# Performance work log

Measured on AMD Instinct MI355X. Metric: run time of the kernel, lower is better.

Reference implementation:

```python
import jax, jax.numpy as jnp
import numpy as np

N, E, D_IN, D_OUT = 100000, 3200000, 128, 128


def setup_inputs() -> dict:
    key = jax.random.key(0)
    ks = jax.random.split(key, 6)
    return {
        "x": jax.random.normal(ks[0], (N, D_IN), dtype=jnp.float32),
        "row": jax.random.randint(ks[1], (E,), 0, N),
        "col": jax.random.randint(ks[2], (E,), 0, N),
        "W0": jax.random.normal(ks[3], (D_OUT, D_IN), dtype=jnp.float32) * (1.0 / np.sqrt(D_IN)),
        "b0": jnp.zeros((D_OUT,), jnp.float32),
        "W1": jax.random.normal(ks[4], (D_OUT, D_IN), dtype=jnp.float32) * (1.0 / np.sqrt(D_IN)),
        "b1": jnp.zeros((D_OUT,), jnp.float32),
        "att": jax.random.normal(ks[5], (2 * D_OUT,), dtype=jnp.float32) * 0.1,
        "scale0": jnp.ones((D_OUT,), jnp.float32),
        "offset0": jnp.zeros((D_OUT,), jnp.float32),
        "scale1": jnp.ones((D_OUT,), jnp.float32),
        "offset1": jnp.zeros((D_OUT,), jnp.float32),
    }


def _norm(f, scale, offset):
    # per-node normalization over feature dim (bias='norm' branch)
    m = jnp.mean(f, axis=1, keepdims=True)
    v = jnp.var(f, axis=1, keepdims=True) + 1e-9
    return (f - m) * scale * jax.lax.rsqrt(v) + offset


def reference(x, row, col, W0, b0, W1, b1, att, scale0, offset0, scale1, offset1):
    d = W0.shape[0]
    # order-0 (self) and order-1 (neighbor) feature transforms, act='relu'
    h0 = jax.nn.relu(x @ W0.T + b0)  # [N, d]
    h1 = jax.nn.relu(x @ W1.T + b1)  # [N, d]
    # unnormalized GAT attention (no softmax), LeakyReLU(0.2)
    a_self = jax.nn.leaky_relu(h0 @ att[:d], negative_slope=0.2)   # [N]
    a_neigh = jax.nn.leaky_relu(h1 @ att[d:], negative_slope=0.2)  # [N]
    e = a_self[row] + a_neigh[col]                                 # [E]
    # SpMM: out[i] = sum_{(i,j) in edges} e_ij * h1[j]
    agg = jax.ops.segment_sum(e[:, None] * h1[col], row, num_segments=h0.shape[0])
    # batch-norm style normalization per head, then mean-aggregate over orders
    out = _norm(h0, scale0, offset0) + _norm(agg, scale1, offset1)
    return out
```

## Files before the change

kernel.cpp:

```cpp
#include <hip/hip_runtime.h>
#include <hip/hip_bf16.h>

constexpr int D = 128;
constexpr int BUCKET_SHIFT = 7;
constexpr int BUCKET_CAP_LOG2 = 13;
constexpr int BUCKET_CAP = 1 << BUCKET_CAP_LOG2;
typedef __hip_bfloat16 bf16;

__global__ __launch_bounds__(256) void k_gemm(
    const float* __restrict__ x,
    const float* __restrict__ W0, const float* __restrict__ b0,
    const float* __restrict__ W1, const float* __restrict__ b1,
    const float* __restrict__ att,
    float* __restrict__ h0, bf16* __restrict__ h1b,
    float* __restrict__ a_self, float* __restrict__ a_neigh, int N)
{
  constexpr int XS_STRIDE = 132;
  constexpr int WS_STRIDE = 68;
  __shared__ float xs_t[64 * XS_STRIDE];
  __shared__ float ws_t[64 * WS_STRIDE];

  const int t  = threadIdx.x;
  const int nb = blockIdx.x;
  const int fb = blockIdx.y;
  const int n0 = nb * 128;

  const float* __restrict__ W    = (fb < 2) ? W0 : W1;
  const float* __restrict__ bias = (fb < 2) ? b0 : b1;
  float* __restrict__ adest      = (fb < 2) ? a_self : a_neigh;
  const int frow0 = (fb & 1) * 64;

  const int tf = t & 15;
  const int tn = t >> 4;

  const int x_nq = t >> 1;
  const int x_kq = t & 1;
  const int w_f  = t >> 2;
  const int w_kq = t & 3;

  float acc[8][4];
#pragma unroll
  for (int i = 0; i < 8; ++i)
#pragma unroll
    for (int j = 0; j < 4; ++j) acc[i][j] = 0.0f;

  const bool x_ok = (n0 + x_nq) < N;
  const float* xrow = x + (size_t)(n0 + x_nq) * D;
  const float* wrow = W + (size_t)(frow0 + w_f) * D;

  for (int c = 0; c < 2; ++c) {
    const int k0 = c * 64;
    if (c) __syncthreads();

#pragma unroll
    for (int i = 0; i < 8; ++i) {
      const int k = x_kq * 32 + i * 4;
      float4 v = x_ok ? *reinterpret_cast<const float4*>(xrow + k0 + k)
                      : make_float4(0.f, 0.f, 0.f, 0.f);
      xs_t[(k + 0) * XS_STRIDE + x_nq] = v.x;
      xs_t[(k + 1) * XS_STRIDE + x_nq] = v.y;
      xs_t[(k + 2) * XS_STRIDE + x_nq] = v.z;
      xs_t[(k + 3) * XS_STRIDE + x_nq] = v.w;
    }
#pragma unroll
    for (int i = 0; i < 4; ++i) {
      const int k = w_kq * 4 + i * 16;
      float4 v = *reinterpret_cast<const float4*>(wrow + k0 + k);
      ws_t[(k + 0) * WS_STRIDE + w_f] = v.x;
      ws_t[(k + 1) * WS_STRIDE + w_f] = v.y;
      ws_t[(k + 2) * WS_STRIDE + w_f] = v.z;
      ws_t[(k + 3) * WS_STRIDE + w_f] = v.w;
    }
    __syncthreads();

#pragma unroll 4
    for (int k = 0; k < 64; ++k) {
      const float4 a0 = *reinterpret_cast<const float4*>(&xs_t[k * XS_STRIDE + tn * 4]);
      const float4 a1 = *reinterpret_cast<const float4*>(&xs_t[k * XS_STRIDE + 64 + tn * 4]);
      const float4 bvec = *reinterpret_cast<const float4*>(&ws_t[k * WS_STRIDE + tf * 4]);
      const float av[8] = {a0.x, a0.y, a0.z, a0.w, a1.x, a1.y, a1.z, a1.w};
      const float bv[4] = {bvec.x, bvec.y, bvec.z, bvec.w};
#pragma unroll
      for (int i = 0; i < 8; ++i)
#pragma unroll
        for (int j = 0; j < 4; ++j)
          acc[i][j] = fmaf(av[i], bv[j], acc[i][j]);
    }
  }

  const float4 b4 = *reinterpret_cast<const float4*>(&bias[frow0 + tf * 4]);
  const float4 at4 = *reinterpret_cast<const float4*>(
      &att[(fb < 2 ? 0 : 128) + frow0 + tf * 4]);
#pragma unroll
  for (int i = 0; i < 8; ++i) {
    const int nq = (i < 4) ? (tn * 4 + i) : (64 + tn * 4 + (i - 4));
    const int node = n0 + nq;
    float4 r;
    r.x = fmaxf(acc[i][0] + b4.x, 0.0f);
    r.y = fmaxf(acc[i][1] + b4.y, 0.0f);
    r.z = fmaxf(acc[i][2] + b4.z, 0.0f);
    r.w = fmaxf(acc[i][3] + b4.w, 0.0f);
    float pdot = r.x * at4.x + r.y * at4.y + r.z * at4.z + r.w * at4.w;
#pragma unroll
    for (int m2 = 1; m2 < 16; m2 <<= 1) pdot += __shfl_xor(pdot, m2, 16);
    if (node < N) {
      if (fb < 2) {
        *reinterpret_cast<float4*>(&h0[(size_t)node * D + frow0 + tf * 4]) = r;
      } else {
        bf16 p[4] = {__float2bfloat16(r.x), __float2bfloat16(r.y),
                     __float2bfloat16(r.z), __float2bfloat16(r.w)};
        *reinterpret_cast<ushort4*>(&h1b[(size_t)node * D + frow0 + tf * 4]) =
            *reinterpret_cast<const ushort4*>(p);
      }
      if (tf == 0) atomicAdd(&adest[node], pdot);
    }
  }
}

__global__ __launch_bounds__(512) void k_binA(
    const int* __restrict__ row, const int* __restrict__ col,
    int* __restrict__ bukCnt, unsigned* __restrict__ buf1, int E, int NBUK)
{
  constexpr int EPB = 16384;
  __shared__ int hist[1024];
  __shared__ int base[1024];
  const int t = threadIdx.x;
  const int e0 = blockIdx.x * EPB;
  const int e1 = min(e0 + EPB, E);

  for (int i = t; i < 1024; i += 512) hist[i] = 0;
  __syncthreads();
  for (int e = e0 + t; e < e1; e += 512)
    atomicAdd(&hist[row[e] >> BUCKET_SHIFT], 1);
  __syncthreads();
  for (int bk = t; bk < NBUK; bk += 512) {
    int c = hist[bk];
    base[bk] = (c > 0) ? atomicAdd(&bukCnt[bk], c) : 0;
  }
  __syncthreads();
  for (int i = t; i < 1024; i += 512) hist[i] = 0;
  __syncthreads();
  for (int e = e0 + t; e < e1; e += 512) {
    int r = row[e];
    int c = col[e];
    int bk = r >> BUCKET_SHIFT;
    int pos = base[bk] + atomicAdd(&hist[bk], 1);
    if (pos < BUCKET_CAP)
      buf1[((size_t)bk << BUCKET_CAP_LOG2) + pos] =
          ((unsigned)c << BUCKET_SHIFT) | (unsigned)(r & 127);
  }
}

__global__ __launch_bounds__(1024) void k_scanB(
    const int* __restrict__ bukCnt, int* __restrict__ bukBase, int NBUK)
{
  __shared__ int sd[1024];
  const int t = threadIdx.x;
  const int v = (t < NBUK) ? min(bukCnt[t], BUCKET_CAP) : 0;
  sd[t] = v;
  __syncthreads();
  for (int d2 = 1; d2 < 1024; d2 <<= 1) {
    int o = (t >= d2) ? sd[t - d2] : 0;
    __syncthreads();
    sd[t] += o;
    __syncthreads();
  }
  if (t < NBUK) bukBase[t] = sd[t] - v;
}

__global__ __launch_bounds__(256) void k_fine(
    const unsigned* __restrict__ buf1,
    const int* __restrict__ bukCnt, const int* __restrict__ bukBase,
    int* __restrict__ offs, int* __restrict__ cnt,
    int* __restrict__ colS, int N)
{
  __shared__ int lhist[128], lbase[128], lcur[128];
  __shared__ int sd[256];
  const int b = blockIdx.x;
  const int t = threadIdx.x;
  const int rstart = b << BUCKET_SHIFT;
  const int n = min(bukCnt[b], BUCKET_CAP);
  const unsigned* src = buf1 + ((size_t)b << BUCKET_CAP_LOG2);

  if (t < 128) lhist[t] = 0;
  __syncthreads();
  for (int i = t; i < n; i += 256) atomicAdd(&lhist[src[i] & 127u], 1);
  __syncthreads();
  const int v = (t < 128) ? lhist[t] : 0;
  sd[t] = v;
  __syncthreads();
  for (int d2 = 1; d2 < 128; d2 <<= 1) {
    int o = (t >= d2) ? sd[t - d2] : 0;
    __syncthreads();
    sd[t] += o;
    __syncthreads();
  }
  if (t < 128) {
    const int gbase = bukBase[b] + (sd[t] - v);
    lbase[t] = gbase;
    lcur[t] = 0;
    const int r = rstart + t;
    if (r < N) { offs[r] = gbase; cnt[r] = v; }
  }
  __syncthreads();
  for (int i = t; i < n; i += 256) {
    unsigned w = src[i];
    int r = (int)(w & 127u);
    int pos = lbase[r] + atomicAdd(&lcur[r], 1);
    colS[pos] = (int)(w >> BUCKET_SHIFT);
  }
}

__global__ __launch_bounds__(128) void k_agg(
    const float* __restrict__ h0, const bf16* __restrict__ h1b,
    const float* __restrict__ a_self, const float* __restrict__ a_neigh,
    const int* __restrict__ offs, const int* __restrict__ cnt,
    const int* __restrict__ colS,
    const float* __restrict__ scale0, const float* __restrict__ offset0,
    const float* __restrict__ scale1, const float* __restrict__ offset1,
    float* __restrict__ out, int N)
{
  constexpr int CHUNK = 128;
  __shared__ int2  je[CHUNK];
  __shared__ float red[4];
  __shared__ float aggs[128];
  const int i = blockIdx.x;
  const int d = threadIdx.x;
  const int w = d >> 6;
  const int l = d & 63;

  const float h0v = h0[(size_t)i * D + d];

  float a = h0v, b = h0v * h0v;
#pragma unroll
  for (int o = 32; o; o >>= 1) { a += __shfl_down(a, o, 64); b += __shfl_down(b, o, 64); }
  if ((d & 63) == 0) { red[d >> 6] = a; red[2 + (d >> 6)] = b; }
  __syncthreads();
  const float sum0 = red[0] + red[1], sq0 = red[2] + red[3];

  const int start = offs[i];
  const int deg = cnt[i];
  const float asr = a_self[i];
  const float asv = asr > 0.0f ? asr : 0.2f * asr;

  float acc0 = 0.0f, acc1 = 0.0f;
  const char* h1base = reinterpret_cast<const char*>(h1b) + l * 4;

  for (int c0 = 0; c0 < deg; c0 += CHUNK) {
    const int m = min(CHUNK, deg - c0);
    __syncthreads();
    if (d < m) {
      int j = colS[start + c0 + d];
      float an = a_neigh[j];
      an = an > 0.0f ? an : 0.2f * an;
      je[d] = make_int2(j << 8, __float_as_int(asv + an));
    }
    __syncthreads();
    int k = w;
    for (; k + 6 < m; k += 8) {
      int2 p0 = je[k], p1 = je[k + 2], p2 = je[k + 4], p3 = je[k + 6];
      unsigned u0 = *reinterpret_cast<const unsigned*>(h1base + p0.x);
      unsigned u1 = *reinterpret_cast<const unsigned*>(h1base + p1.x);
      unsigned u2 = *reinterpret_cast<const unsigned*>(h1base + p2.x);
      unsigned u3 = *reinterpret_cast<const unsigned*>(h1base + p3.x);
      float w0 = __int_as_float(p0.y), w1 = __int_as_float(p1.y);
      float w2 = __int_as_float(p2.y), w3 = __int_as_float(p3.y);
      acc0 = fmaf(w0, __uint_as_float(u0 << 16), acc0);
      acc1 = fmaf(w0, __uint_as_float(u0 & 0xffff0000u), acc1);
      acc0 = fmaf(w1, __uint_as_float(u1 << 16), acc0);
      acc1 = fmaf(w1, __uint_as_float(u1 & 0xffff0000u), acc1);
      acc0 = fmaf(w2, __uint_as_float(u2 << 16), acc0);
      acc1 = fmaf(w2, __uint_as_float(u2 & 0xffff0000u), acc1);
      acc0 = fmaf(w3, __uint_as_float(u3 << 16), acc0);
      acc1 = fmaf(w3, __uint_as_float(u3 & 0xffff0000u), acc1);
    }
    for (; k < m; k += 2) {
      int2 p = je[k];
      unsigned u = *reinterpret_cast<const unsigned*>(h1base + p.x);
      float wg = __int_as_float(p.y);
      acc0 = fmaf(wg, __uint_as_float(u << 16), acc0);
      acc1 = fmaf(wg, __uint_as_float(u & 0xffff0000u), acc1);
    }
  }

  if (w == 0) *reinterpret_cast<float2*>(&aggs[2 * l]) = make_float2(acc0, acc1);
  __syncthreads();
  if (w == 1) {
    float2 p = *reinterpret_cast<float2*>(&aggs[2 * l]);
    *reinterpret_cast<float2*>(&aggs[2 * l]) = make_float2(p.x + acc0, p.y + acc1);
  }
  __syncthreads();
  const float agg = aggs[d];

  float a1 = agg, b1 = agg * agg;
#pragma unroll
  for (int o = 32; o; o >>= 1) { a1 += __shfl_down(a1, o, 64); b1 += __shfl_down(b1, o, 64); }
  __syncthreads();
  if ((d & 63) == 0) { red[d >> 6] = a1; red[2 + (d >> 6)] = b1; }
  __syncthreads();
  const float sum1 = red[0] + red[1], sq1 = red[2] + red[3];

  const float inv = 1.0f / 128.0f;
  const float m0 = sum0 * inv;
  const float v0 = sq0 * inv - m0 * m0 + 1e-9f;
  const float m1 = sum1 * inv;
  const float v1 = sq1 * inv - m1 * m1 + 1e-9f;
  const float n0v = (h0v - m0) * scale0[d] * rsqrtf(v0) + offset0[d];
  const float n1v = (agg - m1) * scale1[d] * rsqrtf(v1) + offset1[d];
  out[(size_t)i * D + d] = n0v + n1v;
}

extern "C" void kernel_launch(void* const* d_in, const int* in_sizes, int n_in,
                              void* d_out, int out_size, void* d_ws, size_t ws_size,
                              hipStream_t stream)
{
  const float* x       = (const float*)d_in[0];
  const int*   row     = (const int*)d_in[1];
  const int*   col     = (const int*)d_in[2];
  const float* W0      = (const float*)d_in[3];
  const float* b0      = (const float*)d_in[4];
  const float* W1      = (const float*)d_in[5];
  const float* b1      = (const float*)d_in[6];
  const float* att     = (const float*)d_in[7];
  const float* scale0  = (const float*)d_in[8];
  const float* offset0 = (const float*)d_in[9];
  const float* scale1  = (const float*)d_in[10];
  const float* offset1 = (const float*)d_in[11];

  const int N = in_sizes[0] / D;
  const int E = in_sizes[1];
  const int NBUK = (N + 127) >> BUCKET_SHIFT;

  char* ws = (char*)d_ws;
  size_t off = 0;
  auto alloc = [&](size_t bytes) -> void* {
    void* p = ws + off;
    off += (bytes + 511) & ~size_t(511);
    return p;
  };

  float*    h0      = (float*)d_out;
  bf16*     h1b     = (bf16*)alloc((size_t)N * D * sizeof(bf16));
  float*    a_self  = (float*)alloc((size_t)N * sizeof(float));
  float*    a_neigh = (float*)alloc((size_t)N * sizeof(float));
  int*      cnt     = (int*)alloc((size_t)N * sizeof(int));
  int*      offs    = (int*)alloc((size_t)N * sizeof(int));
  int*      bukCnt  = (int*)alloc((size_t)NBUK * sizeof(int));
  int*      bukBase = (int*)alloc((size_t)NBUK * sizeof(int));
  unsigned* buf1    = (unsigned*)alloc(((size_t)NBUK << BUCKET_CAP_LOG2) * sizeof(unsigned));
  int*      colS    = (int*)alloc((size_t)E * sizeof(int));

  hipMemsetAsync(a_self, 0, (size_t)N * sizeof(float), stream);
  hipMemsetAsync(a_neigh, 0, (size_t)N * sizeof(float), stream);
  hipMemsetAsync(bukCnt, 0, (size_t)NBUK * sizeof(int), stream);

  dim3 ggrid((N + 127) / 128, 4);
  k_gemm<<<ggrid, 256, 0, stream>>>(x, W0, b0, W1, b1, att, h0, h1b,
                                    a_self, a_neigh, N);
  const int NBLKA = (E + 16383) / 16384;
  k_binA<<<NBLKA, 512, 0, stream>>>(row, col, bukCnt, buf1, E, NBUK);
  k_scanB<<<1, 1024, 0, stream>>>(bukCnt, bukBase, NBUK);
  k_fine<<<NBUK, 256, 0, stream>>>(buf1, bukCnt, bukBase, offs, cnt, colS, N);
  k_agg<<<N, 128, 0, stream>>>(h0, h1b, a_self, a_neigh, offs, cnt, colS,
                               scale0, offset0, scale1, offset1, (float*)d_out, N);
}
```

Measured before the change: 331.4 us.

## Sort edges into row-by-column-segment runs and aggregate 64 rows per block

Edges are now bucketed per 64 rows and sub-binned by row group, column segment and row, so each wave walks runs of edges whose source columns fall in the same region of h1. One block handles 64 nodes and accumulates their sums in shared memory, then does the per-node normalization with wave shuffles. The goal is better cache locality in the h1 gather and less per-node launch and sync overhead. LeakyReLU on a_neigh moves into a separate small kernel. The cost is that each wave walks its 16 rows serially, adding latency, and the larger bucket count needs a multi-pass scan.

```diff
diff --git a/kernel.cpp b/kernel.cpp
--- a/kernel.cpp
+++ b/kernel.cpp
@@ -2,9 +2,14 @@
 #include <hip/hip_bf16.h>
 
 constexpr int D = 128;
-constexpr int BUCKET_SHIFT = 7;
-constexpr int BUCKET_CAP_LOG2 = 13;
+constexpr int BUCKET_SHIFT = 6;
+constexpr int BUCKET_CAP_LOG2 = 12;
 constexpr int BUCKET_CAP = 1 << BUCKET_CAP_LOG2;
+constexpr int SEG_SHIFT = 13;
+constexpr int NSEG = 13;
+constexpr int BINS_PER_BUCKET = 4 * NSEG * 16;
+constexpr int BINS_PER_WAVE = NSEG * 16;
+constexpr int ROWSTRIDE = 130;
 typedef __hip_bfloat16 bf16;
 
 __global__ __launch_bounds__(256) void k_gemm(
@@ -117,18 +122,24 @@
   }
 }
 
+__global__ void k_lrelu(float* __restrict__ a, int n)
+{
+  int i = blockIdx.x * 256 + threadIdx.x;
+  if (i < n) { float v = a[i]; a[i] = v > 0.f ? v : 0.2f * v; }
+}
+
 __global__ __launch_bounds__(512) void k_binA(
     const int* __restrict__ row, const int* __restrict__ col,
     int* __restrict__ bukCnt, unsigned* __restrict__ buf1, int E, int NBUK)
 {
   constexpr int EPB = 16384;
-  __shared__ int hist[1024];
-  __shared__ int base[1024];
+  __shared__ int hist[1600];
+  __shared__ int base[1600];
   const int t = threadIdx.x;
   const int e0 = blockIdx.x * EPB;
   const int e1 = min(e0 + EPB, E);
 
-  for (int i = t; i < 1024; i += 512) hist[i] = 0;
+  for (int i = t; i < NBUK; i += 512) hist[i] = 0;
   __syncthreads();
   for (int e = e0 + t; e < e1; e += 512)
     atomicAdd(&hist[row[e] >> BUCKET_SHIFT], 1);
@@ -138,7 +149,7 @@
     base[bk] = (c > 0) ? atomicAdd(&bukCnt[bk], c) : 0;
   }
   __syncthreads();
-  for (int i = t; i < 1024; i += 512) hist[i] = 0;
+  for (int i = t; i < NBUK; i += 512) hist[i] = 0;
   __syncthreads();
   for (int e = e0 + t; e < e1; e += 512) {
     int r = row[e];
@@ -147,167 +158,171 @@
     int pos = base[bk] + atomicAdd(&hist[bk], 1);
     if (pos < BUCKET_CAP)
       buf1[((size_t)bk << BUCKET_CAP_LOG2) + pos] =
-          ((unsigned)c << BUCKET_SHIFT) | (unsigned)(r & 127);
+          ((unsigned)c << BUCKET_SHIFT) | (unsigned)(r & 63);
   }
 }
 
 __global__ __launch_bounds__(1024) void k_scanB(
-    const int* __restrict__ bukCnt, int* __restrict__ bukBase, int NBUK)
+    const int* __restrict__ bukCnt, int* __restrict__ bukBase,
+    int* __restrict__ runs, int NBUK)
 {
   __shared__ int sd[1024];
+  __shared__ int carry;
   const int t = threadIdx.x;
-  const int v = (t < NBUK) ? min(bukCnt[t], BUCKET_CAP) : 0;
-  sd[t] = v;
-  __syncthreads();
-  for (int d2 = 1; d2 < 1024; d2 <<= 1) {
-    int o = (t >= d2) ? sd[t - d2] : 0;
-    __syncthreads();
-    sd[t] += o;
-    __syncthreads();
-  }
-  if (t < NBUK) bukBase[t] = sd[t] - v;
+  if (t == 0) carry = 0;
+  __syncthreads();
+  for (int r = 0; r * 1024 < NBUK; ++r) {
+    const int idx = r * 1024 + t;
+    const int v = (idx < NBUK) ? min(bukCnt[idx], BUCKET_CAP) : 0;
+    sd[t] = v;
+    __syncthreads();
+    for (int d2 = 1; d2 < 1024; d2 <<= 1) {
+      int o = (t >= d2) ? sd[t - d2] : 0;
+      __syncthreads();
+      sd[t] += o;
+      __syncthreads();
+    }
+    const int c0 = carry;
+    if (idx < NBUK) bukBase[idx] = c0 + sd[t] - v;
+    __syncthreads();
+    if (t == 1023) carry = c0 + sd[1023];
+    __syncthreads();
+  }
+  if (t == 0) runs[(size_t)NBUK * BINS_PER_BUCKET] = carry;
 }
 
 __global__ __launch_bounds__(256) void k_fine(
     const unsigned* __restrict__ buf1,
     const int* __restrict__ bukCnt, const int* __restrict__ bukBase,
-    int* __restrict__ offs, int* __restrict__ cnt,
-    int* __restrict__ colS, int N)
-{
-  __shared__ int lhist[128], lbase[128], lcur[128];
+    int* __restrict__ runs, int* __restrict__ colS)
+{
+  __shared__ int lhist[BINS_PER_BUCKET], labs[BINS_PER_BUCKET], lcur[BINS_PER_BUCKET];
   __shared__ int sd[256];
   const int b = blockIdx.x;
   const int t = threadIdx.x;
-  const int rstart = b << BUCKET_SHIFT;
   const int n = min(bukCnt[b], BUCKET_CAP);
   const unsigned* src = buf1 + ((size_t)b << BUCKET_CAP_LOG2);
 
-  if (t < 128) lhist[t] = 0;
-  __syncthreads();
-  for (int i = t; i < n; i += 256) atomicAdd(&lhist[src[i] & 127u], 1);
-  __syncthreads();
-  const int v = (t < 128) ? lhist[t] : 0;
-  sd[t] = v;
-  __syncthreads();
-  for (int d2 = 1; d2 < 128; d2 <<= 1) {
+  for (int i = t; i < BINS_PER_BUCKET; i += 256) { lhist[i] = 0; lcur[i] = 0; }
+  __syncthreads();
+  for (int i = t; i < n; i += 256) {
+    unsigned e = src[i];
+    int r = e & 63, c = e >> BUCKET_SHIFT;
+    int bin = (((r >> 4) * NSEG) + (c >> SEG_SHIFT)) * 16 + (r & 15);
+    atomicAdd(&lhist[bin], 1);
+  }
+  __syncthreads();
+  int v[4], s = 0;
+  const int bin0 = t * 4;
+#pragma unroll
+  for (int i = 0; i < 4; ++i) {
+    v[i] = (bin0 + i < BINS_PER_BUCKET) ? lhist[bin0 + i] : 0;
+    s += v[i];
+  }
+  sd[t] = s;
+  __syncthreads();
+  for (int d2 = 1; d2 < 256; d2 <<= 1) {
     int o = (t >= d2) ? sd[t - d2] : 0;
     __syncthreads();
     sd[t] += o;
     __syncthreads();
   }
-  if (t < 128) {
-    const int gbase = bukBase[b] + (sd[t] - v);
-    lbase[t] = gbase;
-    lcur[t] = 0;
-    const int r = rstart + t;
-    if (r < N) { offs[r] = gbase; cnt[r] = v; }
+  int excl = sd[t] - s;
+  const int gb = bukBase[b];
+#pragma unroll
+  for (int i = 0; i < 4; ++i) {
+    if (bin0 + i < BINS_PER_BUCKET) {
+      labs[bin0 + i] = gb + excl;
+      runs[(size_t)b * BINS_PER_BUCKET + bin0 + i] = gb + excl;
+    }
+    excl += v[i];
   }
   __syncthreads();
   for (int i = t; i < n; i += 256) {
-    unsigned w = src[i];
-    int r = (int)(w & 127u);
-    int pos = lbase[r] + atomicAdd(&lcur[r], 1);
-    colS[pos] = (int)(w >> BUCKET_SHIFT);
-  }
-}
-
-__global__ __launch_bounds__(128) void k_agg(
+    unsigned e = src[i];
+    int r = e & 63, c = e >> BUCKET_SHIFT;
+    int bin = (((r >> 4) * NSEG) + (c >> SEG_SHIFT)) * 16 + (r & 15);
+    int pos = labs[bin] + atomicAdd(&lcur[bin], 1);
+    colS[pos] = c;
+  }
+}
+
+__global__ __launch_bounds__(256) void k_agg(
     const float* __restrict__ h0, const bf16* __restrict__ h1b,
     const float* __restrict__ a_self, const float* __restrict__ a_neigh,
-    const int* __restrict__ offs, const int* __restrict__ cnt,
-    const int* __restrict__ colS,
+    const int* __restrict__ runs, const int* __restrict__ colS,
     const float* __restrict__ scale0, const float* __restrict__ offset0,
     const float* __restrict__ scale1, const float* __restrict__ offset1,
     float* __restrict__ out, int N)
 {
-  constexpr int CHUNK = 128;
-  __shared__ int2  je[CHUNK];
-  __shared__ float red[4];
-  __shared__ float aggs[128];
-  const int i = blockIdx.x;
-  const int d = threadIdx.x;
-  const int w = d >> 6;
-  const int l = d & 63;
-
-  const float h0v = h0[(size_t)i * D + d];
-
-  float a = h0v, b = h0v * h0v;
-#pragma unroll
-  for (int o = 32; o; o >>= 1) { a += __shfl_down(a, o, 64); b += __shfl_down(b, o, 64); }
-  if ((d & 63) == 0) { red[d >> 6] = a; red[2 + (d >> 6)] = b; }
-  __syncthreads();
-  const float sum0 = red[0] + red[1], sq0 = red[2] + red[3];
-
-  const int start = offs[i];
-  const int deg = cnt[i];
-  const float asr = a_self[i];
-  const float asv = asr > 0.0f ? asr : 0.2f * asr;
-
-  float acc0 = 0.0f, acc1 = 0.0f;
-  const char* h1base = reinterpret_cast<const char*>(h1b) + l * 4;
-
-  for (int c0 = 0; c0 < deg; c0 += CHUNK) {
-    const int m = min(CHUNK, deg - c0);
-    __syncthreads();
-    if (d < m) {
-      int j = colS[start + c0 + d];
-      float an = a_neigh[j];
-      an = an > 0.0f ? an : 0.2f * an;
-      je[d] = make_int2(j << 8, __float_as_int(asv + an));
-    }
-    __syncthreads();
-    int k = w;
-    for (; k + 6 < m; k += 8) {
-      int2 p0 = je[k], p1 = je[k + 2], p2 = je[k + 4], p3 = je[k + 6];
-      unsigned u0 = *reinterpret_cast<const unsigned*>(h1base + p0.x);
-      unsigned u1 = *reinterpret_cast<const unsigned*>(h1base + p1.x);
-      unsigned u2 = *reinterpret_cast<const unsigned*>(h1base + p2.x);
-      unsigned u3 = *reinterpret_cast<const unsigned*>(h1base + p3.x);
-      float w0 = __int_as_float(p0.y), w1 = __int_as_float(p1.y);
-      float w2 = __int_as_float(p2.y), w3 = __int_as_float(p3.y);
-      acc0 = fmaf(w0, __uint_as_float(u0 << 16), acc0);
-      acc1 = fmaf(w0, __uint_as_float(u0 & 0xffff0000u), acc1);
-      acc0 = fmaf(w1, __uint_as_float(u1 << 16), acc0);
-      acc1 = fmaf(w1, __uint_as_float(u1 & 0xffff0000u), acc1);
-      acc0 = fmaf(w2, __uint_as_float(u2 << 16), acc0);
-      acc1 = fmaf(w2, __uint_as_float(u2 & 0xffff0000u), acc1);
-      acc0 = fmaf(w3, __uint_as_float(u3 << 16), acc0);
-      acc1 = fmaf(w3, __uint_as_float(u3 & 0xffff0000u), acc1);
-    }
-    for (; k < m; k += 2) {
-      int2 p = je[k];
-      unsigned u = *reinterpret_cast<const unsigned*>(h1base + p.x);
-      float wg = __int_as_float(p.y);
-      acc0 = fmaf(wg, __uint_as_float(u << 16), acc0);
-      acc1 = fmaf(wg, __uint_as_float(u & 0xffff0000u), acc1);
-    }
-  }
-
-  if (w == 0) *reinterpret_cast<float2*>(&aggs[2 * l]) = make_float2(acc0, acc1);
-  __syncthreads();
-  if (w == 1) {
-    float2 p = *reinterpret_cast<float2*>(&aggs[2 * l]);
-    *reinterpret_cast<float2*>(&aggs[2 * l]) = make_float2(p.x + acc0, p.y + acc1);
-  }
-  __syncthreads();
-  const float agg = aggs[d];
-
-  float a1 = agg, b1 = agg * agg;
-#pragma unroll
-  for (int o = 32; o; o >>= 1) { a1 += __shfl_down(a1, o, 64); b1 += __shfl_down(b1, o, 64); }
-  __syncthreads();
-  if ((d & 63) == 0) { red[d >> 6] = a1; red[2 + (d >> 6)] = b1; }
-  __syncthreads();
-  const float sum1 = red[0] + red[1], sq1 = red[2] + red[3];
-
+  __shared__ float aggL[64 * ROWSTRIDE];
+  __shared__ int runsL[BINS_PER_BUCKET + 1];
+  __shared__ float asL[64];
+  const int b = blockIdx.x;
+  const int t = threadIdx.x;
+  const int w = t >> 6, l = t & 63;
+  const int rbase = b << 6;
+
+  for (int i = t; i < 64 * ROWSTRIDE; i += 256) aggL[i] = 0.f;
+  for (int i = t; i < BINS_PER_BUCKET + 1; i += 256)
+    runsL[i] = runs[(size_t)b * BINS_PER_BUCKET + i];
+  if (t < 64) {
+    float v = (rbase + t < N) ? a_self[rbase + t] : 0.f;
+    asL[t] = v > 0.f ? v : 0.2f * v;
+  }
+  __syncthreads();
+
+  const char* h1c = reinterpret_cast<const char*>(h1b) + l * 4;
+  const int qbase = w * BINS_PER_WAVE;
+  int cur = runsL[qbase];
+  for (int q = 0; q < BINS_PER_WAVE; ++q) {
+    const int nxt = runsL[qbase + q + 1];
+    if (nxt > cur) {
+      const int rloc = q & 15;
+      const float as = asL[(w << 4) + rloc];
+      float acc0 = 0.f, acc1 = 0.f;
+      for (int e = cur; e < nxt; ++e) {
+        const int j = colS[e];
+        const float an = a_neigh[j];
+        const unsigned u = *reinterpret_cast<const unsigned*>(h1c + ((size_t)j << 8));
+        const float wgt = as + an;
+        acc0 = fmaf(wgt, __uint_as_float(u << 16), acc0);
+        acc1 = fmaf(wgt, __uint_as_float(u & 0xffff0000u), acc1);
+      }
+      float* p = &aggL[((w << 4) + rloc) * ROWSTRIDE + 2 * l];
+      const float2 old = *reinterpret_cast<const float2*>(p);
+      *reinterpret_cast<float2*>(p) = make_float2(old.x + acc0, old.y + acc1);
+    }
+    cur = nxt;
+  }
+  __syncthreads();
+
+  const float2 sc0 = *reinterpret_cast<const float2*>(&scale0[2 * l]);
+  const float2 of0 = *reinterpret_cast<const float2*>(&offset0[2 * l]);
+  const float2 sc1 = *reinterpret_cast<const float2*>(&scale1[2 * l]);
+  const float2 of1 = *reinterpret_cast<const float2*>(&offset1[2 * l]);
   const float inv = 1.0f / 128.0f;
-  const float m0 = sum0 * inv;
-  const float v0 = sq0 * inv - m0 * m0 + 1e-9f;
-  const float m1 = sum1 * inv;
-  const float v1 = sq1 * inv - m1 * m1 + 1e-9f;
-  const float n0v = (h0v - m0) * scale0[d] * rsqrtf(v0) + offset0[d];
-  const float n1v = (agg - m1) * scale1[d] * rsqrtf(v1) + offset1[d];
-  out[(size_t)i * D + d] = n0v + n1v;
+  for (int i = 0; i < 16; ++i) {
+    const int node = rbase + (w << 4) + i;
+    if (node >= N) break;
+    const float2 hv = *reinterpret_cast<const float2*>(&h0[(size_t)node * D + 2 * l]);
+    const float2 av = *reinterpret_cast<const float2*>(
+        &aggL[((w << 4) + i) * ROWSTRIDE + 2 * l]);
+    float sh = hv.x + hv.y, qh = hv.x * hv.x + hv.y * hv.y;
+    float sa = av.x + av.y, qa = av.x * av.x + av.y * av.y;
+#pragma unroll
+    for (int o = 32; o; o >>= 1) {
+      sh += __shfl_xor(sh, o, 64); qh += __shfl_xor(qh, o, 64);
+      sa += __shfl_xor(sa, o, 64); qa += __shfl_xor(qa, o, 64);
+    }
+    const float m0 = sh * inv, v0 = qh * inv - m0 * m0 + 1e-9f;
+    const float m1 = sa * inv, v1 = qa * inv - m1 * m1 + 1e-9f;
+    const float r0 = rsqrtf(v0), r1 = rsqrtf(v1);
+    float2 o2;
+    o2.x = (hv.x - m0) * sc0.x * r0 + of0.x + (av.x - m1) * sc1.x * r1 + of1.x;
+    o2.y = (hv.y - m0) * sc0.y * r0 + of0.y + (av.y - m1) * sc1.y * r1 + of1.y;
+    *reinterpret_cast<float2*>(&out[(size_t)node * D + 2 * l]) = o2;
+  }
 }
 
 extern "C" void kernel_launch(void* const* d_in, const int* in_sizes, int n_in,
@@ -329,7 +344,7 @@
 
   const int N = in_sizes[0] / D;
   const int E = in_sizes[1];
-  const int NBUK = (N + 127) >> BUCKET_SHIFT;
+  const int NBUK = (N + 63) >> BUCKET_SHIFT;
 
   char* ws = (char*)d_ws;
   size_t off = 0;
@@ -343,10 +358,9 @@
   bf16*     h1b     = (bf16*)alloc((size_t)N * D * sizeof(bf16));
   float*    a_self  = (float*)alloc((size_t)N * sizeof(float));
   float*    a_neigh = (float*)alloc((size_t)N * sizeof(float));
-  int*      cnt     = (int*)alloc((size_t)N * sizeof(int));
-  int*      offs    = (int*)alloc((size_t)N * sizeof(int));
   int*      bukCnt  = (int*)alloc((size_t)NBUK * sizeof(int));
   int*      bukBase = (int*)alloc((size_t)NBUK * sizeof(int));
+  int*      runsT   = (int*)alloc(((size_t)NBUK * BINS_PER_BUCKET + 1) * sizeof(int));
   unsigned* buf1    = (unsigned*)alloc(((size_t)NBUK << BUCKET_CAP_LOG2) * sizeof(unsigned));
   int*      colS    = (int*)alloc((size_t)E * sizeof(int));
 
@@ -359,8 +373,10 @@
                                     a_self, a_neigh, N);
   const int NBLKA = (E + 16383) / 16384;
   k_binA<<<NBLKA, 512, 0, stream>>>(row, col, bukCnt, buf1, E, NBUK);
-  k_scanB<<<1, 1024, 0, stream>>>(bukCnt, bukBase, NBUK);
-  k_fine<<<NBUK, 256, 0, stream>>>(buf1, bukCnt, bukBase, offs, cnt, colS, N);
-  k_agg<<<N, 128, 0, stream>>>(h0, h1b, a_self, a_neigh, offs, cnt, colS,
-                               scale0, offset0, scale1, offset1, (float*)d_out, N);
-}
+  k_scanB<<<1, 1024, 0, stream>>>(bukCnt, bukBase, runsT, NBUK);
+  k_fine<<<NBUK, 256, 0, stream>>>(buf1, bukCnt, bukBase, runsT, colS);
+  k_lrelu<<<(N + 255) / 256, 256, 0, stream>>>(a_neigh, N);
+  k_agg<<<NBUK, 256, 0, stream>>>(h0, h1b, a_self, a_neigh, runsT, colS,
+                                  scale0, offset0, scale1, offset1,
+                                  (float*)d_out, N);
+}
```

Result: slower. 757.4 us (+128.5%).
